# Optimization experiments

Measured on AMD Instinct MI355X. Metric: run time of the kernel, lower is better.

The kernel has to match this reference:

```python
import jax, jax.numpy as jnp
import numpy as np

K_MAX, K_MIN = 12.0, 1.0
TEMP = 1.0
STE_ALPHA = 12.0
EPS = 1e-8

DIM, HID, KHID, WHID = 512, 2048, 128, 128
B, N = 8, 1024


def setup_inputs() -> dict:
    key = jax.random.key(0)
    ks = jax.random.split(key, 13)
    def lin(k, fan_in, shape):
        bound = 1.0 / np.sqrt(fan_in)
        return jax.random.uniform(k, shape, jnp.float32, -bound, bound)
    return {
        "x": jax.random.normal(ks[0], (B, N, DIM), jnp.float32),
        "fc1_w": lin(ks[1], DIM, (HID, DIM)),
        "fc1_b": lin(ks[2], DIM, (HID,)),
        "fc2_w": lin(ks[3], HID, (DIM, HID)),
        "fc2_b": lin(ks[4], HID, (DIM,)),
        "k1_w": lin(ks[5], DIM, (KHID, DIM)),
        "k1_b": lin(ks[6], DIM, (KHID,)),
        "k2_w": lin(ks[7], KHID, (3, KHID)),
        "k2_b": lin(ks[8], KHID, (3,)),
        "w1_w": lin(ks[9], DIM, (WHID, DIM)),
        "w1_b": lin(ks[10], DIM, (WHID,)),
        "w2_w": lin(ks[11], WHID, (3, WHID)),
        "w2_b": lin(ks[12], WHID, (3,)),
    }


def adaptive_knn_aggregate(h, k_cont):
    # h: (B,N,C), k_cont: (B,) continuous k in [k_min, k_max]
    sim = jnp.einsum("bnc,bmc->bnm", h, h) / TEMP          # (B,N,N)
    order = jnp.argsort(-sim, axis=-1)                      # descending
    rank = jnp.argsort(order, axis=-1).astype(h.dtype)      # rank 0 = most similar
    # soft top-k gate (STE-style sigmoid around k_cont)
    gate = jax.nn.sigmoid(STE_ALPHA * (k_cont[:, None, None] - (rank + 0.5)))
    attn = jax.nn.softmax(sim, axis=-1) * gate
    attn = attn / (attn.sum(axis=-1, keepdims=True) + EPS)
    return jnp.einsum("bnm,bmc->bnc", attn, h)


def reference(x, fc1_w, fc1_b, fc2_w, fc2_b, k1_w, k1_b, k2_w, k2_b,
              w1_w, w1_b, w2_w, w2_b):
    pooled = x.mean(axis=1)                                 # (B,C)
    # adaptive k values net
    kh = jax.nn.relu(pooled @ k1_w.T + k1_b)
    ratio = jax.nn.sigmoid(kh @ k2_w.T + k2_b)              # (B,3)
    k_cont = K_MIN + ratio * (K_MAX - K_MIN)
    # adaptive branch weights net
    wh = jax.nn.relu(pooled @ w1_w.T + w1_b)
    w = jax.nn.softmax(wh @ w2_w.T + w2_b, axis=-1)         # (B,3)
    # MLP (dropout p=0 -> identity)
    h = jax.nn.relu(x @ fc1_w.T + fc1_b)
    h = h @ fc2_w.T + fc2_b                                 # (B,N,C)
    # three KNN aggregation branches blended by w
    y = sum(adaptive_knn_aggregate(h, k_cont[:, i]) * w[:, i, None, None]
            for i in range(3))
    return y
```

## Files before the change

### kernel.cpp

```cpp
#include <hip/hip_runtime.h>
#include <math.h>

#define DIM_ 512
#define HID_ 2048
#define B_ 8
#define N_ 1024
#define ROWS_ 8192
#define TOPK 16

typedef __attribute__((ext_vector_type(8))) short short8;
typedef __attribute__((ext_vector_type(16))) float float16v;

__device__ __forceinline__ float sigm(float x) { return 1.f / (1.f + __expf(-x)); }

__device__ __forceinline__ short f2bf(float f) {
    unsigned u = __float_as_uint(f);
    u += 0x7FFF + ((u >> 16) & 1);
    return (short)(u >> 16);
}

__device__ __forceinline__ float bf2f(unsigned short s) {
    return __uint_as_float((unsigned)s << 16);
}

__device__ __forceinline__ unsigned f2ord(float f) {
    unsigned u = __float_as_uint(f);
    return (u & 0x80000000u) ? ~u : (u | 0x80000000u);
}

__device__ __forceinline__ void gload16(const short* g, short* l) {
    __builtin_amdgcn_global_load_lds(
        (const __attribute__((address_space(1))) void*)g,
        (__attribute__((address_space(3))) void*)l, 16, 0, 0);
}

__global__ __launch_bounds__(512)
void prep_kernel(const float* __restrict__ x, float* __restrict__ part, short* __restrict__ xb,
                 const float* __restrict__ w1, const float* __restrict__ w2,
                 short* __restrict__ o1, short* __restrict__ o2) {
    const int bx = blockIdx.x;
    if (bx < 256) {
        const int b = bx >> 5, chunk = bx & 31;
        const int c = threadIdx.x;
        const long long base = ((long long)b * N_ + chunk * 32) * DIM_ + c;
        const float* xp = x + base;
        short* xo = xb + base;
        float s = 0.f;
        for (int n = 0; n < 32; ++n) {
            const float v = xp[(long long)n * DIM_];
            s += v;
            xo[(long long)n * DIM_] = f2bf(v);
        }
        part[(long long)bx * DIM_ + c] = s;
    } else {
        const int n4 = HID_ * DIM_ / 4;
        int i = (bx - 256) * 2048 + threadIdx.x;
#pragma unroll
        for (int t = 0; t < 4; ++t, i += 512) {
            const float* in = (i < n4) ? w1 : w2;
            short* out = (i < n4) ? o1 : o2;
            const int j = (i < n4) ? i : (i - n4);
            const float4 v = *(const float4*)(in + (long long)j * 4);
            short4 o;
            o.x = f2bf(v.x); o.y = f2bf(v.y); o.z = f2bf(v.z); o.w = f2bf(v.w);
            *(short4*)(out + (long long)j * 4) = o;
        }
    }
}

__global__ __launch_bounds__(512)
void pool_heads_kernel(const float* __restrict__ part,
                       const float* __restrict__ k1w, const float* __restrict__ k1b,
                       const float* __restrict__ k2w, const float* __restrict__ k2b,
                       const float* __restrict__ w1w, const float* __restrict__ w1b,
                       const float* __restrict__ w2w, const float* __restrict__ w2b,
                       float* __restrict__ kcont, float* __restrict__ wbr) {
    const int b = blockIdx.x;
    const int t = threadIdx.x;
    __shared__ float sp[DIM_];
    __shared__ float kh[128], wh[128];
    __shared__ float wraw[4];
    float s = 0.f;
    for (int g = 0; g < 32; ++g) s += part[((long long)b * 32 + g) * DIM_ + t];
    sp[t] = s * (1.f / 1024.f);
    __syncthreads();
    if (t < 128) {
        float ak = k1b[t], aw = w1b[t];
        for (int k = 0; k < DIM_; ++k) {
            const float pv = sp[k];
            ak = fmaf(pv, k1w[t * DIM_ + k], ak);
            aw = fmaf(pv, w1w[t * DIM_ + k], aw);
        }
        kh[t] = fmaxf(ak, 0.f);
        wh[t] = fmaxf(aw, 0.f);
    }
    __syncthreads();
    if (t < 3) {
        float rk = k2b[t], rw = w2b[t];
        for (int k = 0; k < 128; ++k) {
            rk = fmaf(kh[k], k2w[t * 128 + k], rk);
            rw = fmaf(wh[k], w2w[t * 128 + k], rw);
        }
        kcont[b * 3 + t] = 1.f + 11.f * sigm(rk);
        wraw[t] = rw;
    }
    __syncthreads();
    if (t == 0) {
        const float m = fmaxf(wraw[0], fmaxf(wraw[1], wraw[2]));
        const float e0 = __expf(wraw[0] - m), e1 = __expf(wraw[1] - m), e2 = __expf(wraw[2] - m);
        const float inv = 1.f / (e0 + e1 + e2);
        wbr[b * 3 + 0] = e0 * inv;
        wbr[b * 3 + 1] = e1 * inv;
        wbr[b * 3 + 2] = e2 * inv;
    }
}

template<int OUTMODE, int BN, int SWZ>
__global__ __launch_bounds__(256)
void gemm_mfma(const short* __restrict__ A, const short* __restrict__ Bm,
               const float* __restrict__ bias,
               float* __restrict__ outF, short* __restrict__ outB,
               int M, int N, int K, int lda, int ldb,
               long long sA, long long sB, long long sC) {
    constexpr int NJ = BN / 64;
    int bz, mi, ni;
    if (SWZ == 1) {
        const int id = blockIdx.x + gridDim.x * (blockIdx.y + gridDim.y * blockIdx.z);
        bz = id % gridDim.z;
        const int r = id / gridDim.z;
        ni = r % gridDim.x;
        mi = r / gridDim.x;
    } else {
        const int id = blockIdx.x + gridDim.x * blockIdx.y;
        const int numM = gridDim.y;
        const int mg = numM >> 3;
        bz = blockIdx.z;
        mi = (id & 7) * mg + (id >> 3) % mg;
        ni = id / numM;
    }
    A  += (long long)bz * sA;
    Bm += (long long)bz * sB;

    __shared__ short As[128 * 64];
    __shared__ short Bs[BN * 64];

    const int tid = threadIdx.x;
    const int lane = tid & 63;
    const int wv = tid >> 6;
    const int m0 = mi * 128;
    const int n0 = ni * BN;

    const int lrow = lane >> 3;
    const int cg = (lane & 7) ^ lrow;

    const int ml = (wv & 1) * 64;
    const int nl = (wv >> 1) * (BN / 2);
    const int fr = lane & 31;
    const int khh = lane >> 5;

    float16v acc[2][NJ];
#pragma unroll
    for (int i = 0; i < 2; ++i)
#pragma unroll
        for (int j = 0; j < NJ; ++j)
#pragma unroll
            for (int r = 0; r < 16; ++r) acc[i][j][r] = 0.f;

    for (int k0 = 0; k0 < K; k0 += 64) {
        __syncthreads();
#pragma unroll
        for (int i = 0; i < 4; ++i) {
            const int rloc = wv * 32 + i * 8 + lrow;
            gload16(A + (long long)(m0 + rloc) * lda + (k0 + cg * 8),
                    &As[(wv * 32 + i * 8) * 64]);
        }
#pragma unroll
        for (int i = 0; i < BN / 32; ++i) {
            const int rloc = wv * (BN / 4) + i * 8 + lrow;
            gload16(Bm + (long long)(n0 + rloc) * ldb + (k0 + cg * 8),
                    &Bs[(wv * (BN / 4) + i * 8) * 64]);
        }
        __syncthreads();
#pragma unroll
        for (int c = 0; c < 4; ++c) {
            const int ch = c * 2 + khh;
            short8 af[2], bfr[NJ];
#pragma unroll
            for (int i = 0; i < 2; ++i) {
                const int m = ml + i * 32 + fr;
                af[i] = *(const short8*)&As[m * 64 + ((ch ^ (m & 7)) * 8)];
            }
#pragma unroll
            for (int j = 0; j < NJ; ++j) {
                const int n = nl + j * 32 + fr;
                bfr[j] = *(const short8*)&Bs[n * 64 + ((ch ^ (n & 7)) * 8)];
            }
#pragma unroll
            for (int i = 0; i < 2; ++i)
#pragma unroll
                for (int j = 0; j < NJ; ++j)
                    acc[i][j] = __builtin_amdgcn_mfma_f32_32x32x16_bf16(
                        af[i], bfr[j], acc[i][j], 0, 0, 0);
        }
    }

    const long long outOfs = (long long)bz * sC;
#pragma unroll
    for (int i = 0; i < 2; ++i) {
#pragma unroll
        for (int j = 0; j < NJ; ++j) {
            const int ng = n0 + nl + j * 32 + fr;
            float bv = 0.f;
            if (OUTMODE != 2) bv = bias[ng];
#pragma unroll
            for (int r = 0; r < 16; ++r) {
                const int mg2 = m0 + ml + i * 32 + (r & 3) + 8 * (r >> 2) + 4 * khh;
                float v = acc[i][j][r] + bv;
                if (OUTMODE == 0) v = fmaxf(v, 0.f);
                const long long idx = outOfs + (long long)mg2 * N + ng;
                if (OUTMODE == 2) outF[idx] = v;
                else              outB[idx] = f2bf(v);
            }
        }
    }
}

__global__ __launch_bounds__(256)
void topk_agg_kernel(const float* __restrict__ sim,
                     const float* __restrict__ kcont, const float* __restrict__ wbr,
                     const unsigned short* __restrict__ h, float* __restrict__ y) {
    const int wv = threadIdx.x >> 6;
    const int lane = threadIdx.x & 63;
    const int ll = lane & 15;
    const int id = blockIdx.x;
    const int b = id & 7;
    const int row0 = b * N_ + (id >> 3) * 8 + wv * 2;
    const float* srowA = sim + (long long)row0 * N_;
    const float* srowB = srowA + N_;

    const int base = lane * 16;
    float fA[16], fB[16];
#pragma unroll
    for (int q = 0; q < 4; ++q) {
        const float4 va = *(const float4*)(srowA + base + q * 4);
        const float4 vb = *(const float4*)(srowB + base + q * 4);
        fA[q * 4 + 0] = va.x; fA[q * 4 + 1] = va.y; fA[q * 4 + 2] = va.z; fA[q * 4 + 3] = va.w;
        fB[q * 4 + 0] = vb.x; fB[q * 4 + 1] = vb.y; fB[q * 4 + 2] = vb.z; fB[q * 4 + 3] = vb.w;
    }

    float mA = fA[0], mB = fB[0];
#pragma unroll
    for (int j = 1; j < 16; ++j) { mA = fmaxf(mA, fA[j]); mB = fmaxf(mB, fB[j]); }
#pragma unroll
    for (int d = 32; d > 0; d >>= 1) {
        mA = fmaxf(mA, __shfl_xor(mA, d));
        mB = fmaxf(mB, __shfl_xor(mB, d));
    }
    const float maxvA = mA, maxvB = mB;

    float sAo = 0.f, sBo = 0.f;
#pragma unroll
    for (int j = 0; j < 16; ++j) { sAo += __expf(fA[j] - maxvA); sBo += __expf(fB[j] - maxvB); }
#pragma unroll
    for (int d = 32; d > 0; d >>= 1) {
        sAo += __shfl_xor(sAo, d);
        sBo += __shfl_xor(sBo, d);
    }
    const float invdenA = 1.f / sAo, invdenB = 1.f / sBo;

    unsigned keyA[16], keyB[16];
#pragma unroll
    for (int j = 0; j < 16; ++j) {
        keyA[j] = (f2ord(fA[j]) & 0xFFFFFC00u) | (unsigned)(1023 - (base + j));
        keyB[j] = (f2ord(fB[j]) & 0xFFFFFC00u) | (unsigned)(1023 - (base + j));
    }

#pragma unroll
    for (int k = 2; k <= 16; k <<= 1) {
#pragma unroll
        for (int j = k >> 1; j > 0; j >>= 1) {
#pragma unroll
            for (int i = 0; i < 16; ++i) {
                const int l = i ^ j;
                if (l > i) {
                    const bool desc = ((i & k) == 0);
                    {
                        const unsigned a = keyA[i], bk = keyA[l];
                        const unsigned hi = (a > bk) ? a : bk;
                        const unsigned lo = (a > bk) ? bk : a;
                        keyA[i] = desc ? hi : lo;
                        keyA[l] = desc ? lo : hi;
                    }
                    {
                        const unsigned a = keyB[i], bk = keyB[l];
                        const unsigned hi = (a > bk) ? a : bk;
                        const unsigned lo = (a > bk) ? bk : a;
                        keyB[i] = desc ? hi : lo;
                        keyB[l] = desc ? lo : hi;
                    }
                }
            }
        }
    }

#pragma unroll
    for (int d = 1; d < 64; d <<= 1) {
        unsigned oA[16], oB[16];
#pragma unroll
        for (int i = 0; i < 16; ++i) {
            oA[i] = __shfl_xor(keyA[15 - i], d);
            oB[i] = __shfl_xor(keyB[15 - i], d);
        }
#pragma unroll
        for (int i = 0; i < 16; ++i) {
            keyA[i] = (keyA[i] > oA[i]) ? keyA[i] : oA[i];
            keyB[i] = (keyB[i] > oB[i]) ? keyB[i] : oB[i];
        }
#pragma unroll
        for (int j = 8; j > 0; j >>= 1) {
#pragma unroll
            for (int i = 0; i < 16; ++i) {
                if ((i & j) == 0) {
                    {
                        const unsigned a = keyA[i], bk = keyA[i | j];
                        keyA[i]     = (a > bk) ? a : bk;
                        keyA[i | j] = (a > bk) ? bk : a;
                    }
                    {
                        const unsigned a = keyB[i], bk = keyB[i | j];
                        keyB[i]     = (a > bk) ? a : bk;
                        keyB[i | j] = (a > bk) ? bk : a;
                    }
                }
            }
        }
    }

    const int rowSel = (lane >> 4) & 1;
    unsigned k32 = 0;
#pragma unroll
    for (int j = 0; j < 16; ++j) {
        const unsigned sel = rowSel ? keyB[j] : keyA[j];
        k32 = (ll == j) ? sel : k32;
    }
    const int myidx = 1023 - (int)(k32 & 1023u);
    const float* srow = rowSel ? srowB : srowA;
    const float myval = srow[myidx];

    unsigned long long kx = ((unsigned long long)f2ord(myval) << 32)
                          | (unsigned)(1023 - myidx);
#pragma unroll
    for (int k = 2; k <= 16; k <<= 1) {
#pragma unroll
        for (int d = k >> 1; d > 0; d >>= 1) {
            const unsigned long long other = __shfl_xor(kx, d);
            const bool keepMax = (((ll & k) != 0) == ((ll & d) != 0));
            const bool mineBig = (kx > other);
            kx = (keepMax == mineBig) ? kx : other;
        }
    }
    const unsigned sord = (unsigned)(kx >> 32);
    const unsigned su = (sord & 0x80000000u) ? (sord & 0x7FFFFFFFu) : ~sord;
    const float sval = __uint_as_float(su);
    const int sidx = 1023 - (int)(kx & 1023u);

    const float kc0 = kcont[b * 3 + 0], kc1 = kcont[b * 3 + 1], kc2 = kcont[b * 3 + 2];
    const float w0 = wbr[b * 3 + 0], w1 = wbr[b * 3 + 1], w2 = wbr[b * 3 + 2];

    const float mv = rowSel ? maxvB : maxvA;
    const float ivd = rowSel ? invdenB : invdenA;
    const float p = __expf(sval - mv) * ivd;
    const float rr = (float)ll + 0.5f;
    const float g0 = sigm(12.f * (kc0 - rr));
    const float g1 = sigm(12.f * (kc1 - rr));
    const float g2 = sigm(12.f * (kc2 - rr));
    float s0 = p * g0, s1 = p * g1, s2 = p * g2;
#pragma unroll
    for (int d = 1; d < 16; d <<= 1) {
        s0 += __shfl_xor(s0, d);
        s1 += __shfl_xor(s1, d);
        s2 += __shfl_xor(s2, d);
    }
    const float f0 = w0 / (s0 + 1e-8f);
    const float f1 = w1 / (s1 + 1e-8f);
    const float f2 = w2 / (s2 + 1e-8f);
    const float mycoef = p * (f0 * g0 + f1 * g1 + f2 * g2);

    const unsigned short* hbase = h + (long long)b * (N_ * DIM_) + lane * 8;
    float accA[8] = {0.f, 0.f, 0.f, 0.f, 0.f, 0.f, 0.f, 0.f};
    float accB[8] = {0.f, 0.f, 0.f, 0.f, 0.f, 0.f, 0.f, 0.f};
    const int half = lane & 32;
#pragma unroll
    for (int r = 0; r < 16; ++r) {
        const float cA = __shfl(mycoef, half | r);
        const int   iA = __shfl(sidx,  half | r);
        const float cB = __shfl(mycoef, half | 16 | r);
        const int   iB = __shfl(sidx,  half | 16 | r);
        const ushort4 a0 = *(const ushort4*)(hbase + (long long)iA * DIM_);
        const ushort4 a1 = *(const ushort4*)(hbase + (long long)iA * DIM_ + 4);
        const ushort4 b0 = *(const ushort4*)(hbase + (long long)iB * DIM_);
        const ushort4 b1 = *(const ushort4*)(hbase + (long long)iB * DIM_ + 4);
        accA[0] = fmaf(cA, bf2f(a0.x), accA[0]);
        accA[1] = fmaf(cA, bf2f(a0.y), accA[1]);
        accA[2] = fmaf(cA, bf2f(a0.z), accA[2]);
        accA[3] = fmaf(cA, bf2f(a0.w), accA[3]);
        accA[4] = fmaf(cA, bf2f(a1.x), accA[4]);
        accA[5] = fmaf(cA, bf2f(a1.y), accA[5]);
        accA[6] = fmaf(cA, bf2f(a1.z), accA[6]);
        accA[7] = fmaf(cA, bf2f(a1.w), accA[7]);
        accB[0] = fmaf(cB, bf2f(b0.x), accB[0]);
        accB[1] = fmaf(cB, bf2f(b0.y), accB[1]);
        accB[2] = fmaf(cB, bf2f(b0.z), accB[2]);
        accB[3] = fmaf(cB, bf2f(b0.w), accB[3]);
        accB[4] = fmaf(cB, bf2f(b1.x), accB[4]);
        accB[5] = fmaf(cB, bf2f(b1.y), accB[5]);
        accB[6] = fmaf(cB, bf2f(b1.z), accB[6]);
        accB[7] = fmaf(cB, bf2f(b1.w), accB[7]);
    }
    float* ypA = y + (long long)row0 * DIM_ + lane * 8;
    float* ypB = ypA + DIM_;
    *(float4*)(ypA + 0) = make_float4(accA[0], accA[1], accA[2], accA[3]);
    *(float4*)(ypA + 4) = make_float4(accA[4], accA[5], accA[6], accA[7]);
    *(float4*)(ypB + 0) = make_float4(accB[0], accB[1], accB[2], accB[3]);
    *(float4*)(ypB + 4) = make_float4(accB[4], accB[5], accB[6], accB[7]);
}

extern "C" void kernel_launch(void* const* d_in, const int* in_sizes, int n_in,
                              void* d_out, int out_size, void* d_ws, size_t ws_size,
                              hipStream_t stream) {
    const float* x     = (const float*)d_in[0];
    const float* fc1_w = (const float*)d_in[1];
    const float* fc1_b = (const float*)d_in[2];
    const float* fc2_w = (const float*)d_in[3];
    const float* fc2_b = (const float*)d_in[4];
    const float* k1_w  = (const float*)d_in[5];
    const float* k1_b  = (const float*)d_in[6];
    const float* k2_w  = (const float*)d_in[7];
    const float* k2_b  = (const float*)d_in[8];
    const float* w1_w  = (const float*)d_in[9];
    const float* w1_b  = (const float*)d_in[10];
    const float* w2_w  = (const float*)d_in[11];
    const float* w2_b  = (const float*)d_in[12];

    char* ws = (char*)d_ws;
    short* h1b    = (short*)(ws + 0);
    float* simbuf = (float*)(ws + 0);
    short* xb     = (short*)(ws + 33554432);
    short* hb     = (short*)(ws + 67108864);
    short* w1b    = (short*)(ws + 75497472);
    short* w2b    = (short*)(ws + 77594624);
    float* ppart  = (float*)(ws + 79691776);
    float* kcont  = (float*)(ws + 80216064);
    float* wbr    = (float*)(ws + 80216192);

    float* y = (float*)d_out;

    prep_kernel<<<dim3(512), dim3(512), 0, stream>>>(x, ppart, xb, fc1_w, fc2_w, w1b, w2b);
    pool_heads_kernel<<<dim3(B_), dim3(512), 0, stream>>>(ppart, k1_w, k1_b, k2_w, k2_b,
                                                          w1_w, w1_b, w2_w, w2_b, kcont, wbr);
    gemm_mfma<0, 128, 2><<<dim3(HID_ / 128, ROWS_ / 128, 1), dim3(256), 0, stream>>>(
        xb, w1b, fc1_b, nullptr, h1b, ROWS_, HID_, DIM_, DIM_, DIM_, 0, 0, 0);
    gemm_mfma<1, 64, 2><<<dim3(DIM_ / 64, ROWS_ / 128, 1), dim3(256), 0, stream>>>(
        h1b, w2b, fc2_b, nullptr, hb, ROWS_, DIM_, HID_, HID_, HID_, 0, 0, 0);
    gemm_mfma<2, 128, 1><<<dim3(N_ / 128, N_ / 128, B_), dim3(256), 0, stream>>>(
        hb, hb, nullptr, simbuf, nullptr, N_, N_, DIM_, DIM_, DIM_,
        (long long)N_ * DIM_, (long long)N_ * DIM_, (long long)N_ * N_);
    topk_agg_kernel<<<dim3(ROWS_ / 8), dim3(256), 0, stream>>>(
        simbuf, kcont, wbr, (const unsigned short*)hb, y);
}
```

Before: 214.4 us.

## Add 256x256-tile pipelined MFMA GEMM for fc1 and similarity matmuls

```diff
diff --git a/kernel.cpp b/kernel.cpp
--- a/kernel.cpp
+++ b/kernel.cpp
@@ -10,6 +10,7 @@
 
 typedef __attribute__((ext_vector_type(8))) short short8;
 typedef __attribute__((ext_vector_type(16))) float float16v;
+typedef __attribute__((ext_vector_type(4))) float float4v;
 
 __device__ __forceinline__ float sigm(float x) { return 1.f / (1.f + __expf(-x)); }
 
@@ -218,6 +219,144 @@
                 float v = acc[i][j][r] + bv;
                 if (OUTMODE == 0) v = fmaxf(v, 0.f);
                 const long long idx = outOfs + (long long)mg2 * N + ng;
+                if (OUTMODE == 2) outF[idx] = v;
+                else              outB[idx] = f2bf(v);
+            }
+        }
+    }
+}
+
+template<int OUTMODE, bool BATCH>
+__global__ __launch_bounds__(512, 2)
+void gemm256(const short* __restrict__ A, const short* __restrict__ Bm,
+             const float* __restrict__ bias, float* __restrict__ outF,
+             short* __restrict__ outB, int M, int N, int K, int lda, int ldb,
+             int mTiles, long long sA, long long sB, long long sC) {
+    __shared__ short As[2][256 * 64];
+    __shared__ short Bs[2][256 * 64];
+
+    const int tid = threadIdx.x;
+    const int lane = tid & 63;
+    const int wv = tid >> 6;
+    const int l15 = lane & 15;
+    const int kq = lane >> 4;
+    const int lr = lane >> 3;
+    const int cg = (lane & 7) ^ lr;
+
+    const int id = blockIdx.x;
+    const int xcd = id & 7;
+    const int r = id >> 3;
+    int mi, ni;
+    const short* Ag = A;
+    const short* Bg = Bm;
+    long long cOfs = 0;
+    if (BATCH) {
+        mi = r % mTiles; ni = r / mTiles;
+        Ag += (long long)xcd * sA; Bg += (long long)xcd * sB; cOfs = (long long)xcd * sC;
+    } else {
+        const int mg = mTiles >> 3;
+        mi = xcd * mg + r % mg; ni = r / mg;
+    }
+    const int m0 = mi * 256, n0 = ni * 256;
+    const int wm = wv >> 2, wn = wv & 3;
+
+    float4v acc[8][4];
+#pragma unroll
+    for (int i = 0; i < 8; ++i)
+#pragma unroll
+        for (int j = 0; j < 4; ++j)
+#pragma unroll
+            for (int q = 0; q < 4; ++q) acc[i][j][q] = 0.f;
+
+    const int sB1 = (wv & 3) + (wv >> 2) * 8;
+
+    auto stA = [&](int bf, int s, int k0) {
+        gload16(Ag + (long long)(m0 + s * 8 + lr) * lda + (k0 + cg * 8), &As[bf][s * 8 * 64]);
+    };
+    auto stB = [&](int bf, int s, int k0) {
+        gload16(Bg + (long long)(n0 + s * 8 + lr) * ldb + (k0 + cg * 8), &Bs[bf][s * 8 * 64]);
+    };
+    auto unit0 = [&](int bf, int k0) {
+        stA(bf, wv, k0); stA(bf, 16 + wv, k0);
+        stB(bf, sB1, k0); stB(bf, 16 + sB1, k0);
+    };
+    auto unit1 = [&](int bf, int k0) { stA(bf, 8 + wv, k0); stA(bf, 24 + wv, k0); };
+    auto unit2 = [&](int bf, int k0) { stB(bf, 4 + sB1, k0); stB(bf, 20 + sB1, k0); };
+
+    auto tile_body = [&](int bf, int k1, bool stage) {
+#pragma unroll
+        for (int p = 0; p < 4; ++p) {
+            const int mq = p & 1, nq = p >> 1;
+            short8 af[4][2], bfr[2][2];
+#pragma unroll
+            for (int f = 0; f < 4; ++f) {
+                const int rA = wm * 128 + mq * 64 + f * 16 + l15;
+                const int ro = rA * 64, sw = rA & 7;
+#pragma unroll
+                for (int ks = 0; ks < 2; ++ks)
+                    af[f][ks] = *(const short8*)&As[bf][ro + (((ks * 4 + kq) ^ sw) * 8)];
+            }
+#pragma unroll
+            for (int g = 0; g < 2; ++g) {
+                const int rB = wn * 64 + nq * 32 + g * 16 + l15;
+                const int ro = rB * 64, sw = rB & 7;
+#pragma unroll
+                for (int ks = 0; ks < 2; ++ks)
+                    bfr[g][ks] = *(const short8*)&Bs[bf][ro + (((ks * 4 + kq) ^ sw) * 8)];
+            }
+            if (stage) {
+                if (p == 0) unit0(bf ^ 1, k1);
+                else if (p == 1) unit1(bf ^ 1, k1);
+                else if (p == 2) unit2(bf ^ 1, k1);
+                if (p == 0 || p == 1) asm volatile("s_waitcnt vmcnt(6)" ::: "memory");
+                else if (p == 3)      asm volatile("s_waitcnt vmcnt(4)" ::: "memory");
+            } else {
+                if (p == 0)      asm volatile("s_waitcnt vmcnt(2)" ::: "memory");
+                else if (p == 1) asm volatile("s_waitcnt vmcnt(0)" ::: "memory");
+            }
+            __builtin_amdgcn_s_barrier();
+            asm volatile("s_waitcnt lgkmcnt(0)" ::: "memory");
+            __builtin_amdgcn_sched_barrier(0);
+            __builtin_amdgcn_s_setprio(1);
+#pragma unroll
+            for (int f = 0; f < 4; ++f)
+#pragma unroll
+                for (int g = 0; g < 2; ++g)
+#pragma unroll
+                    for (int ks = 0; ks < 2; ++ks)
+                        acc[mq * 4 + f][nq * 2 + g] = __builtin_amdgcn_mfma_f32_16x16x32_bf16(
+                            af[f][ks], bfr[g][ks], acc[mq * 4 + f][nq * 2 + g], 0, 0, 0);
+            __builtin_amdgcn_s_setprio(0);
+            if (stage || p < 3) __builtin_amdgcn_s_barrier();
+        }
+    };
+
+    const int NT = K >> 6;
+    unit0(0, 0);
+    __builtin_amdgcn_sched_barrier(0);
+    unit1(0, 0);
+    __builtin_amdgcn_sched_barrier(0);
+    unit2(0, 0);
+    asm volatile("s_waitcnt vmcnt(4)" ::: "memory");
+    __builtin_amdgcn_s_barrier();
+
+    for (int t = 0; t < NT - 1; ++t)
+        tile_body(t & 1, (t + 1) << 6, true);
+    tile_body((NT - 1) & 1, 0, false);
+
+#pragma unroll
+    for (int mf = 0; mf < 8; ++mf) {
+#pragma unroll
+        for (int nf = 0; nf < 4; ++nf) {
+            const int ng = n0 + wn * 64 + nf * 16 + l15;
+            float bv = 0.f;
+            if (OUTMODE != 2) bv = bias[ng];
+            const int mb = m0 + wm * 128 + mf * 16 + kq * 4;
+#pragma unroll
+            for (int q = 0; q < 4; ++q) {
+                float v = acc[mf][nf][q] + bv;
+                if (OUTMODE == 0) v = fmaxf(v, 0.f);
+                const long long idx = cOfs + (long long)(mb + q) * N + ng;
                 if (OUTMODE == 2) outF[idx] = v;
                 else              outB[idx] = f2bf(v);
             }
@@ -458,12 +597,12 @@
     prep_kernel<<<dim3(512), dim3(512), 0, stream>>>(x, ppart, xb, fc1_w, fc2_w, w1b, w2b);
     pool_heads_kernel<<<dim3(B_), dim3(512), 0, stream>>>(ppart, k1_w, k1_b, k2_w, k2_b,
                                                           w1_w, w1_b, w2_w, w2_b, kcont, wbr);
-    gemm_mfma<0, 128, 2><<<dim3(HID_ / 128, ROWS_ / 128, 1), dim3(256), 0, stream>>>(
-        xb, w1b, fc1_b, nullptr, h1b, ROWS_, HID_, DIM_, DIM_, DIM_, 0, 0, 0);
+    gemm256<0, false><<<dim3(256), dim3(512), 0, stream>>>(
+        xb, w1b, fc1_b, nullptr, h1b, ROWS_, HID_, DIM_, DIM_, DIM_, 32, 0, 0, 0);
     gemm_mfma<1, 64, 2><<<dim3(DIM_ / 64, ROWS_ / 128, 1), dim3(256), 0, stream>>>(
         h1b, w2b, fc2_b, nullptr, hb, ROWS_, DIM_, HID_, HID_, HID_, 0, 0, 0);
-    gemm_mfma<2, 128, 1><<<dim3(N_ / 128, N_ / 128, B_), dim3(256), 0, stream>>>(
-        hb, hb, nullptr, simbuf, nullptr, N_, N_, DIM_, DIM_, DIM_,
+    gemm256<2, true><<<dim3(128), dim3(512), 0, stream>>>(
+        hb, hb, nullptr, simbuf, nullptr, N_, N_, DIM_, DIM_, DIM_, 4,
         (long long)N_ * DIM_, (long long)N_ * DIM_, (long long)N_ * N_);
     topk_agg_kernel<<<dim3(ROWS_ / 8), dim3(256), 0, stream>>>(
         simbuf, kcont, wbr, (const unsigned short*)hb, y);
```

Result: slower. 219.4 us (+2.3%).
